# Performance work log

Hardware: AMD Instinct MI355X
Metric: run time of the kernel (lower is better)

Reference implementation:

```python
import jax, jax.numpy as jnp
import numpy as np

SCALES = (1, 2, 4)
KS = 5          # conv kernel size
POOL = 2        # maxpool kernel & stride


def coarse_grain(x, s):
    # non-overlapping mean pool along last axis
    B, C, L = x.shape
    Lc = L // s
    return x[:, :, : Lc * s].reshape(B, C, Lc, s).mean(axis=-1)


def conv1d(x, w, b):
    # x: [B, C_in, L], w: [C_out, C_in, K] (torch layout), VALID padding, stride 1
    y = jax.lax.conv_general_dilated(
        x, w, window_strides=(1,), padding='VALID',
        dimension_numbers=('NCH', 'OIH', 'NCH'))
    return y + b[None, :, None]


def maxpool1d(x, k):
    B, C, L = x.shape
    Lp = L // k
    return x[:, :, : Lp * k].reshape(B, C, Lp, k).max(axis=-1)


def conv_block(x, w1, b1, w2, b2):
    x = maxpool1d(jax.nn.relu(conv1d(x, w1, b1)), POOL)
    x = maxpool1d(jax.nn.relu(conv1d(x, w2, b2)), POOL)
    return x


def setup_inputs() -> dict:
    key = jax.random.key(0)
    ks = jax.random.split(key, 9)
    B, C, NWL = 2048, 4, 480
    C1, C2 = 16, 32
    # flatten size per model's own arithmetic: sum over scales of conv/pool output lens * C2
    F = (117 + 57 + 27) * C2  # 6432
    NOUT = 5
    sc = lambda fan_in: 1.0 / np.sqrt(fan_in)
    return {
        'x':  jax.random.normal(ks[0], (B, C, NWL), dtype=jnp.float32),
        'w1': jax.random.uniform(ks[1], (C1, C, KS), jnp.float32, -sc(C * KS), sc(C * KS)),
        'b1': jax.random.uniform(ks[2], (C1,), jnp.float32, -sc(C * KS), sc(C * KS)),
        'w2': jax.random.uniform(ks[3], (C2, C1, KS), jnp.float32, -sc(C1 * KS), sc(C1 * KS)),
        'b2': jax.random.uniform(ks[4], (C2,), jnp.float32, -sc(C1 * KS), sc(C1 * KS)),
        'wl': jax.random.uniform(ks[5], (F, F), jnp.float32, -sc(F), sc(F)),
        'bl': jax.random.uniform(ks[6], (F,), jnp.float32, -sc(F), sc(F)),
        'wo': jax.random.uniform(ks[7], (NOUT, F), jnp.float32, -sc(F), sc(F)),
        'bo': jax.random.uniform(ks[8], (NOUT,), jnp.float32, -sc(F), sc(F)),
    }


def reference(x, w1, b1, w2, b2, wl, bl, wo, bo):
    # multi-scale feature mapping: shared ConvBlock applied to each coarse-grained scale
    feats = [conv_block(coarse_grain(x, s), w1, b1, w2, b2) for s in SCALES]
    f = jnp.concatenate(feats, axis=-1)            # [B, 32, 201]
    f = f.reshape(f.shape[0], -1)                  # [B, 6432]
    # the SAME linear layer (shared weights) is applied 4 times in torch
    for _ in range(4):
        f = jax.nn.relu(f @ wl.T + bl)
    return f @ wo.T + bo                           # [B, 5]
```

## Files before the change

kernel.cpp:

```cpp
#include <hip/hip_runtime.h>

typedef _Float16 v8h  __attribute__((ext_vector_type(8)));
typedef _Float16 v4h  __attribute__((ext_vector_type(4)));
typedef float    f32x16 __attribute__((ext_vector_type(16)));

#define GK 6432
#define GN 6432
#define GM 2048
#define KP 6528

__global__ void convert_w(const float* __restrict__ wl, _Float16* __restrict__ Wh)
{
    const int row = blockIdx.y;
    const int col = (blockIdx.x * 256 + threadIdx.x) * 4;
    if (col >= KP) return;
    v4h h;
    if (col < GK) {
        const float4 f = *(const float4*)(wl + (long)row * GK + col);
        h[0] = (_Float16)f.x; h[1] = (_Float16)f.y;
        h[2] = (_Float16)f.z; h[3] = (_Float16)f.w;
    } else {
        h[0] = (_Float16)0.f; h[1] = (_Float16)0.f;
        h[2] = (_Float16)0.f; h[3] = (_Float16)0.f;
    }
    *(v4h*)(Wh + (long)row * KP + col) = h;
}

#define SX   0
#define SX2  2048
#define SX4  3136
#define SW1  3712
#define SB1  4032
#define SW2  4048
#define SB2  6608
#define SP1  6640
#define LDSZ 13808

__global__ __launch_bounds__(256) void conv_feat(
    const float* __restrict__ x,
    const float* __restrict__ w1, const float* __restrict__ b1,
    const float* __restrict__ w2, const float* __restrict__ b2,
    _Float16* __restrict__ F0)
{
    __shared__ float lds[LDSZ];
    const int tid = threadIdx.x;
    const long b  = blockIdx.x;

    for (int i = tid; i < 1920; i += 256) {
        int c = i / 480, t = i % 480;
        lds[SX + c * 512 + t] = x[(b * 4 + c) * 480 + t];
    }
    for (int i = tid; i < 320;  i += 256) lds[SW1 + i] = w1[i];
    for (int i = tid; i < 16;   i += 256) lds[SB1 + i] = b1[i];
    for (int i = tid; i < 2560; i += 256) lds[SW2 + i] = w2[i];
    for (int i = tid; i < 32;   i += 256) lds[SB2 + i] = b2[i];
    for (int i = tid; i < KP - GK; i += 256) F0[b * KP + GK + i] = (_Float16)0.f;
    __syncthreads();

    for (int i = tid; i < 960; i += 256) {
        int c = i / 240, t = i % 240;
        lds[SX2 + c * 272 + t] = 0.5f * (lds[SX + c * 512 + 2 * t] + lds[SX + c * 512 + 2 * t + 1]);
    }
    for (int i = tid; i < 480; i += 256) {
        int c = i / 120, t = i % 120;
        float s = lds[SX + c * 512 + 4 * t]     + lds[SX + c * 512 + 4 * t + 1]
                + lds[SX + c * 512 + 4 * t + 2] + lds[SX + c * 512 + 4 * t + 3];
        lds[SX4 + c * 144 + t] = 0.25f * s;
    }
    __syncthreads();

    for (int jid = tid; jid < 16 * 34; jid += 256) {
        const int c1 = jid / 34, rid = jid % 34;
        const int sidx = (rid < 19) ? 0 : (rid < 29 ? 1 : 2);
        const int r0   = (sidx == 0) ? rid : (sidx == 1 ? rid - 19 : rid - 29);
        const int u0   = r0 * 13;
        const int xbase  = (sidx == 0) ? SX  : (sidx == 1 ? SX2 : SX4);
        const int xpitch = (sidx == 0) ? 512 : (sidx == 1 ? 272 : 144);
        const int P      = (sidx == 0) ? 238 : (sidx == 1 ? 118 : 58);
        const int pofs   = (sidx == 0) ? 0   : (sidx == 1 ? 238 : 356);

        float acc[26];
        const float bias = lds[SB1 + c1];
        #pragma unroll
        for (int i = 0; i < 26; ++i) acc[i] = bias;

        #pragma unroll
        for (int ci = 0; ci < 4; ++ci) {
            float w[30];
            const float* xr = &lds[xbase + ci * xpitch + 2 * u0];
            #pragma unroll
            for (int q = 0; q < 15; ++q) {
                float2 t2 = *(const float2*)(xr + 2 * q);
                w[2 * q] = t2.x; w[2 * q + 1] = t2.y;
            }
            float wt[5];
            #pragma unroll
            for (int k = 0; k < 5; ++k) wt[k] = lds[SW1 + (c1 * 4 + ci) * 5 + k];
            #pragma unroll
            for (int i = 0; i < 26; ++i) {
                #pragma unroll
                for (int k = 0; k < 5; ++k) acc[i] += w[i + k] * wt[k];
            }
        }
        #pragma unroll
        for (int i = 0; i < 13; ++i) {
            int u = u0 + i;
            if (u < P)
                lds[SP1 + c1 * 448 + pofs + u] = fmaxf(fmaxf(acc[2 * i], acc[2 * i + 1]), 0.f);
        }
    }
    __syncthreads();

    for (int jid = tid; jid < 32 * 17; jid += 256) {
        const int c2 = jid / 17, rid = jid % 17;
        const int sidx = (rid < 9) ? 0 : (rid < 14 ? 1 : 2);
        const int r0   = (sidx == 0) ? rid : (sidx == 1 ? rid - 9 : rid - 14);
        const int v0   = r0 * 13;
        const int pbase = (sidx == 0) ? 0   : (sidx == 1 ? 238 : 356);
        const int Pv    = (sidx == 0) ? 117 : (sidx == 1 ? 57  : 27);
        const int vout  = (sidx == 0) ? 0   : (sidx == 1 ? 117 : 174);

        float acc[26];
        const float bias = lds[SB2 + c2];
        #pragma unroll
        for (int i = 0; i < 26; ++i) acc[i] = bias;

        for (int c1 = 0; c1 < 16; ++c1) {
            float w[30];
            const float* pr = &lds[SP1 + c1 * 448 + pbase + 2 * v0];
            #pragma unroll
            for (int q = 0; q < 15; ++q) {
                float2 t2 = *(const float2*)(pr + 2 * q);
                w[2 * q] = t2.x; w[2 * q + 1] = t2.y;
            }
            float wt[5];
            #pragma unroll
            for (int k = 0; k < 5; ++k) wt[k] = lds[SW2 + (c2 * 16 + c1) * 5 + k];
            #pragma unroll
            for (int i = 0; i < 26; ++i) {
                #pragma unroll
                for (int k = 0; k < 5; ++k) acc[i] += w[i + k] * wt[k];
            }
        }
        #pragma unroll
        for (int i = 0; i < 13; ++i) {
            int v = v0 + i;
            if (v < Pv) {
                float f = fmaxf(fmaxf(acc[2 * i], acc[2 * i + 1]), 0.f);
                F0[b * KP + c2 * 201 + vout + v] = (_Float16)f;
            }
        }
    }
}

__global__ __launch_bounds__(512, 2) void gemm8(
    const _Float16* __restrict__ A, const _Float16* __restrict__ Bw,
    const float* __restrict__ bias, _Float16* __restrict__ C)
{
    __shared__ _Float16 sA[2][256 * 64];
    __shared__ _Float16 sB[2][256 * 64];

    const int tid  = threadIdx.x;
    const int lane = tid & 63;
    const int wave = tid >> 6;
    const int wr   = wave >> 2;
    const int wc   = wave & 3;

    const int id  = blockIdx.x;
    const long tile_m = (long)(id & 7) << 8;
    const long tile_n = (long)(id >> 3) << 8;

    const int lrow = lane >> 3;
    const int lcol = ((lane & 7) ^ lrow) << 3;

    const int arow = wr * 128 + wc * 32;
    const int brow = wc * 64 + wr * 32;
    const _Float16* pA = A + (tile_m + arow + lrow) * (long)KP + lcol;
    long br0 = tile_n + brow + lrow;
    long br1 = br0 + 8, br2 = br0 + 16, br3 = br0 + 24;
    if (br0 > 6431) br0 = 6431;
    if (br1 > 6431) br1 = 6431;
    if (br2 > 6431) br2 = 6431;
    if (br3 > 6431) br3 = 6431;
    const _Float16* pB0 = Bw + br0 * (long)KP + lcol;
    const _Float16* pB1 = Bw + br1 * (long)KP + lcol;
    const _Float16* pB2 = Bw + br2 * (long)KP + lcol;
    const _Float16* pB3 = Bw + br3 * (long)KP + lcol;

    const int aDst = arow * 64;
    const int bDst = brow * 64;

#define GLD(p, d) __builtin_amdgcn_global_load_lds(                          \
        (const __attribute__((address_space(1))) void*)(p),                  \
        (__attribute__((address_space(3))) void*)(d), 16, 0, 0)

#define STAGE_A4(SBUF, KO) {                                                 \
    GLD(pA + (KO),            &sA[SBUF][aDst]);                              \
    GLD(pA + (KO) +  8L * KP, &sA[SBUF][aDst +  512]);                       \
    GLD(pA + (KO) + 16L * KP, &sA[SBUF][aDst + 1024]);                       \
    GLD(pA + (KO) + 24L * KP, &sA[SBUF][aDst + 1536]); }

#define STAGE_B4(SBUF, KO) {                                                 \
    GLD(pB0 + (KO), &sB[SBUF][bDst]);                                        \
    GLD(pB1 + (KO), &sB[SBUF][bDst +  512]);                                 \
    GLD(pB2 + (KO), &sB[SBUF][bDst + 1024]);                                 \
    GLD(pB3 + (KO), &sB[SBUF][bDst + 1536]); }

    const int fr32 = lane & 31;
    const int g    = lane >> 5;
    const int sw8  = lane & 7;
    int q8[4];
    #pragma unroll
    for (int s = 0; s < 4; ++s) q8[s] = (((2 * s + g) ^ sw8) << 3);

    const int bS = wc * 64 + wr * 32;
    const int bO = wc * 64 + (1 - wr) * 32;

    v8h af[2][4], bfS[4], bfO[4];
    f32x16 accS[4], accO[4];
    #pragma unroll
    for (int f = 0; f < 4; ++f) {
        #pragma unroll
        for (int r = 0; r < 16; ++r) { accS[f][r] = 0.f; accO[f][r] = 0.f; }
    }

#define LDA(CA, H) { _Pragma("unroll")                                       \
    for (int j = 0; j < 2; ++j) { _Pragma("unroll")                          \
        for (int s = 0; s < 4; ++s)                                          \
            af[j][s] = *(const v8h*)&(CA)[(wr * 128 + ((H) * 2 + j) * 32 + fr32) * 64 + q8[s]]; \
    } }

#define LDBF(CB, BROW, D) { _Pragma("unroll")                                \
    for (int s = 0; s < 4; ++s)                                              \
        D[s] = *(const v8h*)&(CB)[((BROW) + fr32) * 64 + q8[s]]; }

#define MMAP(A0, A1, BF) { _Pragma("unroll")                                 \
    for (int s = 0; s < 4; ++s) {                                            \
        A0 = __builtin_amdgcn_mfma_f32_32x32x16_f16(af[0][s], BF[s], A0, 0, 0, 0); \
        A1 = __builtin_amdgcn_mfma_f32_32x32x16_f16(af[1][s], BF[s], A1, 0, 0, 0); \
    } }

#define ROUND(CA, CB, SBUF, KO, S2) {                                        \
                             \
    LDBF(CB, bS, bfS); LDA(CA, 0);                                           \
    __builtin_amdgcn_s_barrier();                                            \
    asm volatile("s_waitcnt lgkmcnt(0)" ::: "memory");                       \
    __builtin_amdgcn_s_setprio(1);                                           \
    MMAP(accS[0], accS[1], bfS);                                             \
    __builtin_amdgcn_s_setprio(0);                                           \
    __builtin_amdgcn_s_barrier();                                            \
                      \
    LDBF(CB, bO, bfO);                                                       \
    if ((S2) && wc < 2) STAGE_A4(SBUF, KO);                                  \
    __builtin_amdgcn_s_barrier();                                            \
    asm volatile("s_waitcnt lgkmcnt(0)" ::: "memory");                       \
    __builtin_amdgcn_s_setprio(1);                                           \
    MMAP(accO[0], accO[1], bfO);                                             \
    __builtin_amdgcn_s_setprio(0);                                           \
    __builtin_amdgcn_s_barrier();                                            \
                       \
    LDA(CA, 1);                                                              \
    if (S2) STAGE_B4(SBUF, KO);                                              \
    __builtin_amdgcn_s_barrier();                                            \
    asm volatile("s_waitcnt lgkmcnt(0)" ::: "memory");                       \
    __builtin_amdgcn_s_setprio(1);                                           \
    MMAP(accO[2], accO[3], bfO);                                             \
    __builtin_amdgcn_s_setprio(0);                                           \
    __builtin_amdgcn_s_barrier();                                            \
                \
    if ((S2) && wc >= 2) STAGE_A4(SBUF, KO);                                 \
    __builtin_amdgcn_s_barrier();                                            \
    __builtin_amdgcn_s_setprio(1);                                           \
    MMAP(accS[2], accS[3], bfS);                                             \
    __builtin_amdgcn_s_setprio(0);                                           \
    if (S2) { asm volatile("s_waitcnt vmcnt(8)" ::: "memory"); }             \
    else    { asm volatile("s_waitcnt vmcnt(0)" ::: "memory"); }             \
    __builtin_amdgcn_s_barrier(); }

    STAGE_A4(0, 0);  STAGE_B4(0, 0);
    STAGE_A4(1, 64); STAGE_B4(1, 64);
    pA += 128; pB0 += 128; pB1 += 128; pB2 += 128; pB3 += 128;
    asm volatile("s_waitcnt vmcnt(8)" ::: "memory");
    __builtin_amdgcn_s_barrier();

    for (int kt = 0; kt < 102; kt += 2) {
        ROUND(sA[0], sB[0], 0, 0,  kt < 100);
        ROUND(sA[1], sB[1], 1, 64, kt < 99);
        pA += 128; pB0 += 128; pB1 += 128; pB2 += 128; pB3 += 128;
    }

#define EPI(ACC, COL) {                                                      \
    const bool val   = (COL) < GN;                                           \
    const bool wr_ok = (COL) < KP;                                           \
    const float bv = val ? bias[COL] : 0.f;                                  \
    if (wr_ok) { _Pragma("unroll")                                           \
        for (int f = 0; f < 4; ++f) { _Pragma("unroll")                      \
            for (int r = 0; r < 16; ++r) {                                   \
                const long row = tile_m + wr * 128 + f * 32                  \
                               + (r & 3) + 8 * (r >> 2) + 4 * g;             \
                float v = ACC[f][r] + bv;                                    \
                v = v > 0.f ? v : 0.f;                                       \
                C[row * (long)KP + (COL)] = val ? (_Float16)v : (_Float16)0.f; \
            } } } }

    const long colS = tile_n + bS + fr32;
    const long colO = tile_n + bO + fr32;
    EPI(accS, colS);
    EPI(accO, colO);

#undef GLD
#undef STAGE_A4
#undef STAGE_B4
#undef LDA
#undef LDBF
#undef MMAP
#undef ROUND
#undef EPI
}

__global__ __launch_bounds__(256) void final_out(
    const _Float16* __restrict__ F, const float* __restrict__ wo,
    const float* __restrict__ bo, float* __restrict__ out)
{
    __shared__ float red[4][8];
    const long b   = blockIdx.x;
    const int tid  = threadIdx.x;
    const int lane = tid & 63;
    const int wave = tid >> 6;
    float acc[5] = {0.f, 0.f, 0.f, 0.f, 0.f};
    const _Float16* f = F + b * KP;

    const int c1 = (wave + 1) * 402;
    for (int c = wave * 402 + lane; c < c1; c += 64) {
        const int k = c << 2;
        v4h f4 = *(const v4h*)(f + k);
        const float f0 = (float)f4[0], f1 = (float)f4[1];
        const float f2 = (float)f4[2], f3 = (float)f4[3];
        #pragma unroll
        for (int o = 0; o < 5; ++o) {
            const float4 w4 = *(const float4*)(wo + o * GK + k);
            acc[o] += f0 * w4.x + f1 * w4.y + f2 * w4.z + f3 * w4.w;
        }
    }
    #pragma unroll
    for (int o = 0; o < 5; ++o) {
        #pragma unroll
        for (int off = 32; off > 0; off >>= 1) acc[o] += __shfl_down(acc[o], off, 64);
    }
    if (lane == 0) {
        #pragma unroll
        for (int o = 0; o < 5; ++o) red[wave][o] = acc[o];
    }
    __syncthreads();
    if (tid < 5)
        out[b * 5 + tid] = red[0][tid] + red[1][tid] + red[2][tid] + red[3][tid] + bo[tid];
}

extern "C" void kernel_launch(void* const* d_in, const int* in_sizes, int n_in,
                              void* d_out, int out_size, void* d_ws, size_t ws_size,
                              hipStream_t stream)
{
    const float* x  = (const float*)d_in[0];
    const float* w1 = (const float*)d_in[1];
    const float* b1 = (const float*)d_in[2];
    const float* w2 = (const float*)d_in[3];
    const float* b2 = (const float*)d_in[4];
    const float* wl = (const float*)d_in[5];
    const float* bl = (const float*)d_in[6];
    const float* wo = (const float*)d_in[7];
    const float* bo = (const float*)d_in[8];
    float* out = (float*)d_out;

    char* ws = (char*)d_ws;
    _Float16* Wh = (_Float16*)ws;
    _Float16* F0 = (_Float16*)(ws + 83976192);
    _Float16* F1 = (_Float16*)(ws + 83976192 + 26738688);

    convert_w<<<dim3(7, GN), 256, 0, stream>>>(wl, Wh);
    conv_feat<<<GM, 256, 0, stream>>>(x, w1, b1, w2, b2, F0);
    gemm8<<<208, 512, 0, stream>>>(F0, Wh, bl, F1);
    gemm8<<<208, 512, 0, stream>>>(F1, Wh, bl, F0);
    gemm8<<<208, 512, 0, stream>>>(F0, Wh, bl, F1);
    gemm8<<<208, 512, 0, stream>>>(F1, Wh, bl, F0);
    final_out<<<GM, 256, 0, stream>>>(F0, wo, bo, out);
}
```

Before: 1.176 ms.

## Rewrite GEMM with 16 waves per block and 16x16x32 MFMA tiles

The 256x256 GEMM tile is now computed by 16 waves (1024 threads) instead of 8. Each wave owns a 64x64 sub-tile built from 16x16x32 MFMA instructions rather than 32x32x16 ones. Global-to-LDS staging is redistributed across the waves, and the B stage for the next buffer is issued one round earlier. The aim is to raise in-flight waves and latency hiding within each CU, at the cost of more LDS fragment reads per MFMA, more barrier participants, and lower per-instruction MFMA efficiency.

```diff
diff --git a/kernel.cpp b/kernel.cpp
--- a/kernel.cpp
+++ b/kernel.cpp
@@ -1,8 +1,8 @@
 #include <hip/hip_runtime.h>
 
-typedef _Float16 v8h  __attribute__((ext_vector_type(8)));
-typedef _Float16 v4h  __attribute__((ext_vector_type(4)));
-typedef float    f32x16 __attribute__((ext_vector_type(16)));
+typedef _Float16 v8h __attribute__((ext_vector_type(8)));
+typedef _Float16 v4h __attribute__((ext_vector_type(4)));
+typedef float    v4f __attribute__((ext_vector_type(4)));
 
 #define GK 6432
 #define GN 6432
@@ -153,7 +153,7 @@
     }
 }
 
-__global__ __launch_bounds__(512, 2) void gemm8(
+__global__ __launch_bounds__(1024, 4) void gemm16(
     const _Float16* __restrict__ A, const _Float16* __restrict__ Bw,
     const float* __restrict__ bias, _Float16* __restrict__ C)
 {
@@ -163,159 +163,153 @@
     const int tid  = threadIdx.x;
     const int lane = tid & 63;
     const int wave = tid >> 6;
-    const int wr   = wave >> 2;
-    const int wc   = wave & 3;
-
-    const int id  = blockIdx.x;
+    const int wm   = wave >> 2;
+    const int wn   = wave & 3;
+
+    const int id = blockIdx.x;
     const long tile_m = (long)(id & 7) << 8;
     const long tile_n = (long)(id >> 3) << 8;
 
     const int lrow = lane >> 3;
     const int lcol = ((lane & 7) ^ lrow) << 3;
 
-    const int arow = wr * 128 + wc * 32;
-    const int brow = wc * 64 + wr * 32;
-    const _Float16* pA = A + (tile_m + arow + lrow) * (long)KP + lcol;
-    long br0 = tile_n + brow + lrow;
-    long br1 = br0 + 8, br2 = br0 + 16, br3 = br0 + 24;
-    if (br0 > 6431) br0 = 6431;
-    if (br1 > 6431) br1 = 6431;
-    if (br2 > 6431) br2 = 6431;
-    if (br3 > 6431) br3 = 6431;
-    const _Float16* pB0 = Bw + br0 * (long)KP + lcol;
-    const _Float16* pB1 = Bw + br1 * (long)KP + lcol;
-    const _Float16* pB2 = Bw + br2 * (long)KP + lcol;
-    const _Float16* pB3 = Bw + br3 * (long)KP + lcol;
-
-    const int aDst = arow * 64;
-    const int bDst = brow * 64;
+    const _Float16* pAst = A + (tile_m + wave * 16 + lrow) * (long)KP + lcol;
+    const int dA0 = wave * 16 * 64, dA1 = dA0 + 512;
+
+    const int bRow01 = (wave >> 2) * 64 + (wave & 3) * 8;
+    long rb01 = tile_n + bRow01;
+    long rb23 = rb01 + 32;
+    long r01l = rb01 + lrow; if (r01l > 6431) r01l = 6431;
+    long r23l = rb23 + lrow; if (r23l > 6431) r23l = 6431;
+    const _Float16* pB01 = Bw + r01l * (long)KP + lcol;
+    const _Float16* pB23 = Bw + r23l * (long)KP + lcol;
+    const int dB01 = bRow01 * 64;
+    const int dB23 = dB01 + 32 * 64;
 
 #define GLD(p, d) __builtin_amdgcn_global_load_lds(                          \
         (const __attribute__((address_space(1))) void*)(p),                  \
         (__attribute__((address_space(3))) void*)(d), 16, 0, 0)
 
-#define STAGE_A4(SBUF, KO) {                                                 \
-    GLD(pA + (KO),            &sA[SBUF][aDst]);                              \
-    GLD(pA + (KO) +  8L * KP, &sA[SBUF][aDst +  512]);                       \
-    GLD(pA + (KO) + 16L * KP, &sA[SBUF][aDst + 1024]);                       \
-    GLD(pA + (KO) + 24L * KP, &sA[SBUF][aDst + 1536]); }
-
-#define STAGE_B4(SBUF, KO) {                                                 \
-    GLD(pB0 + (KO), &sB[SBUF][bDst]);                                        \
-    GLD(pB1 + (KO), &sB[SBUF][bDst +  512]);                                 \
-    GLD(pB2 + (KO), &sB[SBUF][bDst + 1024]);                                 \
-    GLD(pB3 + (KO), &sB[SBUF][bDst + 1536]); }
-
-    const int fr32 = lane & 31;
-    const int g    = lane >> 5;
-    const int sw8  = lane & 7;
-    int q8[4];
+#define STAGE_A(CUR, q)   { GLD(q, &sA[CUR][dA0]); GLD((q) + 8L * KP, &sA[CUR][dA1]); }
+#define STAGE_B01(CUR, q) { GLD(q, &sB[CUR][dB01]); }
+#define STAGE_B23(CUR, q) { GLD(q, &sB[CUR][dB23]); }
+
+    const int fr = lane & 15;
+    const int fp = lane >> 4;
+    const int sw = fr & 7;
+    const int slot0 = ((fp)     ^ sw) << 3;
+    const int slot1 = ((fp + 4) ^ sw) << 3;
+    const int arow0 = wm * 64 + fr;
+    const int brow0 = wn * 64 + fr;
+
+    v8h af[4][2], bf0, bf1;
+    v4f acc[4][4];
     #pragma unroll
-    for (int s = 0; s < 4; ++s) q8[s] = (((2 * s + g) ^ sw8) << 3);
-
-    const int bS = wc * 64 + wr * 32;
-    const int bO = wc * 64 + (1 - wr) * 32;
-
-    v8h af[2][4], bfS[4], bfO[4];
-    f32x16 accS[4], accO[4];
-    #pragma unroll
-    for (int f = 0; f < 4; ++f) {
-        #pragma unroll
-        for (int r = 0; r < 16; ++r) { accS[f][r] = 0.f; accO[f][r] = 0.f; }
-    }
-
-#define LDA(CA, H) { _Pragma("unroll")                                       \
-    for (int j = 0; j < 2; ++j) { _Pragma("unroll")                          \
-        for (int s = 0; s < 4; ++s)                                          \
-            af[j][s] = *(const v8h*)&(CA)[(wr * 128 + ((H) * 2 + j) * 32 + fr32) * 64 + q8[s]]; \
+    for (int mi = 0; mi < 4; ++mi) {
+        #pragma unroll
+        for (int nf = 0; nf < 4; ++nf) { v4f z = {0.f, 0.f, 0.f, 0.f}; acc[mi][nf] = z; }
+    }
+
+#define LDAALL(CUR) { _Pragma("unroll")                                      \
+    for (int mi = 0; mi < 4; ++mi) {                                         \
+        af[mi][0] = *(const v8h*)&sA[CUR][(arow0 + mi * 16) * 64 + slot0];   \
+        af[mi][1] = *(const v8h*)&sA[CUR][(arow0 + mi * 16) * 64 + slot1];   \
     } }
 
-#define LDBF(CB, BROW, D) { _Pragma("unroll")                                \
-    for (int s = 0; s < 4; ++s)                                              \
-        D[s] = *(const v8h*)&(CB)[((BROW) + fr32) * 64 + q8[s]]; }
-
-#define MMAP(A0, A1, BF) { _Pragma("unroll")                                 \
-    for (int s = 0; s < 4; ++s) {                                            \
-        A0 = __builtin_amdgcn_mfma_f32_32x32x16_f16(af[0][s], BF[s], A0, 0, 0, 0); \
-        A1 = __builtin_amdgcn_mfma_f32_32x32x16_f16(af[1][s], BF[s], A1, 0, 0, 0); \
+#define LDB(CUR, P) {                                                        \
+    bf0 = *(const v8h*)&sB[CUR][(brow0 + (P) * 16) * 64 + slot0];            \
+    bf1 = *(const v8h*)&sB[CUR][(brow0 + (P) * 16) * 64 + slot1]; }
+
+#define MMAP(P) { _Pragma("unroll")                                          \
+    for (int mi = 0; mi < 4; ++mi) {                                         \
+        acc[mi][P] = __builtin_amdgcn_mfma_f32_16x16x32_f16(af[mi][0], bf0,  \
+                                                            acc[mi][P], 0, 0, 0); \
+        acc[mi][P] = __builtin_amdgcn_mfma_f32_16x16x32_f16(af[mi][1], bf1,  \
+                                                            acc[mi][P], 0, 0, 0); \
     } }
 
-#define ROUND(CA, CB, SBUF, KO, S2) {                                        \
-                             \
-    LDBF(CB, bS, bfS); LDA(CA, 0);                                           \
+#define ROUND(CUR, S1, S2, VN) {                                             \
+              \
+    LDAALL(CUR); LDB(CUR, 0);                                                \
+    if (S1) STAGE_B23((CUR) ^ 1, qB23);                                      \
     __builtin_amdgcn_s_barrier();                                            \
     asm volatile("s_waitcnt lgkmcnt(0)" ::: "memory");                       \
     __builtin_amdgcn_s_setprio(1);                                           \
-    MMAP(accS[0], accS[1], bfS);                                             \
+    MMAP(0);                                                                 \
     __builtin_amdgcn_s_setprio(0);                                           \
     __builtin_amdgcn_s_barrier();                                            \
-                      \
-    LDBF(CB, bO, bfO);                                                       \
-    if ((S2) && wc < 2) STAGE_A4(SBUF, KO);                                  \
+                             \
+    LDB(CUR, 1);                                                             \
+    if (S2) STAGE_A(CUR, qA);                                                \
     __builtin_amdgcn_s_barrier();                                            \
     asm volatile("s_waitcnt lgkmcnt(0)" ::: "memory");                       \
     __builtin_amdgcn_s_setprio(1);                                           \
-    MMAP(accO[0], accO[1], bfO);                                             \
+    MMAP(1);                                                                 \
     __builtin_amdgcn_s_setprio(0);                                           \
     __builtin_amdgcn_s_barrier();                                            \
-                       \
-    LDA(CA, 1);                                                              \
-    if (S2) STAGE_B4(SBUF, KO);                                              \
+                          \
+    LDB(CUR, 2);                                                             \
+    if (S2) STAGE_B01(CUR, qB01);                                            \
     __builtin_amdgcn_s_barrier();                                            \
     asm volatile("s_waitcnt lgkmcnt(0)" ::: "memory");                       \
     __builtin_amdgcn_s_setprio(1);                                           \
-    MMAP(accO[2], accO[3], bfO);                                             \
+    MMAP(2);                                                                 \
     __builtin_amdgcn_s_setprio(0);                                           \
     __builtin_amdgcn_s_barrier();                                            \
-                \
-    if ((S2) && wc >= 2) STAGE_A4(SBUF, KO);                                 \
-    __builtin_amdgcn_s_barrier();                                            \
+                                    \
+    LDB(CUR, 3);                                                             \
+    __builtin_amdgcn_s_barrier();                                            \
+    asm volatile("s_waitcnt lgkmcnt(0)" ::: "memory");                       \
     __builtin_amdgcn_s_setprio(1);                                           \
-    MMAP(accS[2], accS[3], bfS);                                             \
+    MMAP(3);                                                                 \
     __builtin_amdgcn_s_setprio(0);                                           \
-    if (S2) { asm volatile("s_waitcnt vmcnt(8)" ::: "memory"); }             \
-    else    { asm volatile("s_waitcnt vmcnt(0)" ::: "memory"); }             \
-    __builtin_amdgcn_s_barrier(); }
-
-    STAGE_A4(0, 0);  STAGE_B4(0, 0);
-    STAGE_A4(1, 64); STAGE_B4(1, 64);
-    pA += 128; pB0 += 128; pB1 += 128; pB2 += 128; pB3 += 128;
-    asm volatile("s_waitcnt vmcnt(8)" ::: "memory");
+    asm volatile("s_waitcnt vmcnt(" #VN ")" ::: "memory");                   \
+    __builtin_amdgcn_s_barrier();                                            \
+    qA += 64; qB01 += 64; qB23 += 64; }
+
+    STAGE_A(0, pAst); STAGE_B01(0, pB01); STAGE_B23(0, pB23);
+    STAGE_A(1, pAst + 64); STAGE_B01(1, pB01 + 64);
+    asm volatile("s_waitcnt vmcnt(3)" ::: "memory");
     __builtin_amdgcn_s_barrier();
 
-    for (int kt = 0; kt < 102; kt += 2) {
-        ROUND(sA[0], sB[0], 0, 0,  kt < 100);
-        ROUND(sA[1], sB[1], 1, 64, kt < 99);
-        pA += 128; pB0 += 128; pB1 += 128; pB2 += 128; pB3 += 128;
-    }
-
-#define EPI(ACC, COL) {                                                      \
-    const bool val   = (COL) < GN;                                           \
-    const bool wr_ok = (COL) < KP;                                           \
-    const float bv = val ? bias[COL] : 0.f;                                  \
-    if (wr_ok) { _Pragma("unroll")                                           \
-        for (int f = 0; f < 4; ++f) { _Pragma("unroll")                      \
-            for (int r = 0; r < 16; ++r) {                                   \
-                const long row = tile_m + wr * 128 + f * 32                  \
-                               + (r & 3) + 8 * (r >> 2) + 4 * g;             \
-                float v = ACC[f][r] + bv;                                    \
-                v = v > 0.f ? v : 0.f;                                       \
-                C[row * (long)KP + (COL)] = val ? (_Float16)v : (_Float16)0.f; \
-            } } } }
-
-    const long colS = tile_n + bS + fr32;
-    const long colO = tile_n + bO + fr32;
-    EPI(accS, colS);
-    EPI(accO, colO);
+    const _Float16* qA   = pAst + 128;
+    const _Float16* qB01 = pB01 + 128;
+    const _Float16* qB23 = pB23 + 64;
+
+    for (int kt = 0; kt < 100; kt += 2) {
+        ROUND(0, 1, 1, 3);
+        ROUND(1, 1, 1, 3);
+    }
+    ROUND(0, 1, 0, 0);
+    ROUND(1, 0, 0, 0);
+
+    #pragma unroll
+    for (int nf = 0; nf < 4; ++nf) {
+        const long col = tile_n + wn * 64 + nf * 16 + fr;
+        if (col < KP) {
+            const bool val = col < GN;
+            const float bv = val ? bias[col] : 0.f;
+            #pragma unroll
+            for (int mi = 0; mi < 4; ++mi) {
+                const long row = tile_m + wm * 64 + mi * 16 + fp * 4;
+                #pragma unroll
+                for (int r = 0; r < 4; ++r) {
+                    float v = acc[mi][nf][r] + bv;
+                    v = v > 0.f ? v : 0.f;
+                    C[(row + r) * (long)KP + col] = val ? (_Float16)v : (_Float16)0.f;
+                }
+            }
+        }
+    }
 
 #undef GLD
-#undef STAGE_A4
-#undef STAGE_B4
-#undef LDA
-#undef LDBF
+#undef STAGE_A
+#undef STAGE_B01
+#undef STAGE_B23
+#undef LDAALL
+#undef LDB
 #undef MMAP
 #undef ROUND
-#undef EPI
 }
 
 __global__ __launch_bounds__(256) void final_out(
@@ -378,9 +372,9 @@
 
     convert_w<<<dim3(7, GN), 256, 0, stream>>>(wl, Wh);
     conv_feat<<<GM, 256, 0, stream>>>(x, w1, b1, w2, b2, F0);
-    gemm8<<<208, 512, 0, stream>>>(F0, Wh, bl, F1);
-    gemm8<<<208, 512, 0, stream>>>(F1, Wh, bl, F0);
-    gemm8<<<208, 512, 0, stream>>>(F0, Wh, bl, F1);
-    gemm8<<<208, 512, 0, stream>>>(F1, Wh, bl, F0);
+    gemm16<<<208, 1024, 0, stream>>>(F0, Wh, bl, F1);
+    gemm16<<<208, 1024, 0, stream>>>(F1, Wh, bl, F0);
+    gemm16<<<208, 1024, 0, stream>>>(F0, Wh, bl, F1);
+    gemm16<<<208, 1024, 0, stream>>>(F1, Wh, bl, F0);
     final_out<<<GM, 256, 0, stream>>>(F0, wo, bo, out);
 }
```

Result: no change. 1.179 ms (+0.2%).
